# Kernel optimization log

Hardware: AMD Instinct MI355X
Metric: run time of the kernel (lower is better)

## Reference

```python
import jax, jax.numpy as jnp
import numpy as np
import math

LOG_2PI = math.log(2.0 * math.pi)
ETA = 1.0        # Beta(gamma_1=1, gamma_2=eta) stick-breaking prior (gamma buffers at init)
MC_NUM = 4096    # Monte-Carlo samples
T_CLUSTER = 2    # trunc (must be 2: original normalize_factor broadcast requires it)
T_CLS = 2        # classifier DP truncation
DIM = 1024
N = 65536


def mix_weights(b):
    # stick-breaking: pad(b,(0,1),1) * pad(cumprod(1-b),(1,0),1); b: [..., T] -> [..., T+1]
    b1m = jnp.cumprod(1.0 - b, axis=-1)
    ones = jnp.ones((*b.shape[:-1], 1), b.dtype)
    return jnp.concatenate([b, ones], axis=-1) * jnp.concatenate([ones, b1m], axis=-1)


def gauss_log_prob(x, mu, rho):
    # diag Gaussian log-prob summed over feature dim; x [N,D], mu/rho [T,D] -> [N,T]
    std = jnp.log1p(jnp.exp(rho))                      # sigma = log(1+exp(rho))
    inv_var = 1.0 / (std * std)
    const = -0.5 * x.shape[-1] * LOG_2PI - jnp.sum(jnp.log(std), axis=-1)  # [T]
    # 0.5*sum((x-mu)^2/var) expanded as matmuls to avoid an [N,T,D] intermediate
    quad = 0.5 * ((x * x) @ inv_var.T) - x @ (mu * inv_var).T \
           + 0.5 * jnp.sum(mu * mu * inv_var, axis=-1)
    return const - quad


def gauss_entropy(rho):
    # mean over T of diag-Gaussian entropies; rho [T,D] -> scalar
    D = rho.shape[-1]
    std = jnp.log1p(jnp.exp(rho))
    ent = 0.5 * D * (LOG_2PI + 1.0) + jnp.sum(jnp.log(std), axis=-1)  # [T]
    return jnp.mean(ent)


def setup_inputs() -> dict:
    key = jax.random.key(0)
    ks = jax.random.split(key, 5)
    return {
        "x": jax.random.normal(ks[0], (N, DIM), jnp.float32),
        "mu_c": jax.random.normal(ks[1], (T_CLUSTER, DIM), jnp.float32),
        "rho_c": jax.random.normal(ks[2], (T_CLUSTER, DIM), jnp.float32),
        "mu_f": jax.random.normal(ks[3], (T_CLS, DIM), jnp.float32),
        "rho_f": jax.random.normal(ks[4], (T_CLS, DIM), jnp.float32),
    }


def reference(x, mu_c, rho_c, mu_f, rho_f):
    key = jax.random.key(1)
    k1, k2, k3, k4, k5 = jax.random.split(key, 5)

    # ---- D_P_cluster.likelihood(x) ----
    beta_lik = jax.random.beta(k1, 1.0, ETA, (x.shape[0], T_CLUSTER), x.dtype)
    pi_lik = mix_weights(beta_lik)[:, :-1]                 # [N, T]
    ent = gauss_entropy(rho_c)                             # scalar
    log_pdfs = gauss_log_prob(x, mu_c, rho_c)              # [N, T]
    phi = jax.nn.softmax(jnp.log(pi_lik) + ent + log_pdfs, axis=-1)
    neg_likelihood = -jnp.mean(jnp.sum(phi * (ent + log_pdfs), axis=1))

    # ---- MC sampling from the cluster mixture (fused, no Python loop) ----
    betas = jax.random.beta(k2, 1.0, ETA, (MC_NUM, T_CLUSTER), x.dtype)
    w = mix_weights(betas)[:, :-1]                         # [MC, T]
    w = w / jnp.sum(w, axis=1, keepdims=True)              # row-normalize (T==2 makes this exact)
    draws = jax.random.categorical(k3, jnp.log(w), axis=-1)  # [MC] component indices
    eps = jax.random.normal(k4, (MC_NUM, DIM), x.dtype)
    std_c = jnp.log1p(jnp.exp(rho_c))
    mc_samples = mu_c[draws] + std_c[draws] * eps          # [MC, D] reparametrized

    # ---- D_P_clssfy.infer(mc_samples) ----
    beta_inf = jax.random.beta(k5, 1.0, ETA, (MC_NUM, T_CLS), x.dtype)
    pi_inf = mix_weights(beta_inf)[:, :-1]                 # [MC, 2]
    lp_inf = gauss_log_prob(mc_samples, mu_f, rho_f)       # [MC, 2]
    logits = pi_inf * jax.nn.softmax(lp_inf, axis=1)
    return logits, neg_likelihood
```

## Files before the change

kernel.cpp:

```cpp
#include <hip/hip_runtime.h>
#include <stdint.h>

#define LOG2PI_F 1.8378770664093453f
#define D_DIM 1024

typedef float v4f __attribute__((ext_vector_type(4)));

__device__ __forceinline__ uint32_t mix64_32(uint64_t z) {
    z ^= z >> 33; z *= 0xff51afd7ed558ccdULL;
    z ^= z >> 33; z *= 0xc4ceb9fe1a85ec53ULL;
    z ^= z >> 33;
    return (uint32_t)z;
}
__device__ __forceinline__ float unif01(uint32_t stream, uint32_t idx) {
    uint32_t h = mix64_32(((uint64_t)stream << 32) | (uint64_t)idx);
    return (float)(h >> 9) * 0x1p-23f + 0x1p-24f;
}
__device__ __forceinline__ float softplusf(float r) { return log1pf(expf(r)); }

union F4 { v4f v; float f[4]; };

__global__ __launch_bounds__(256) void hdp_lik_kernel(
    const float* __restrict__ x, const float* __restrict__ mu_c,
    const float* __restrict__ rho_c, double* __restrict__ partial)
{
    __shared__ float H0[D_DIM], A0[D_DIM], H1[D_DIM], A1[D_DIM];
    __shared__ float wred[4][4];
    __shared__ double wpart[4];
    const int tid = threadIdx.x, wid = tid >> 6, lane = tid & 63;

    float sls0 = 0.f, sls1 = 0.f, bq0 = 0.f, bq1 = 0.f;
    {
        const int d = tid * 4;
        F4 r0, r1, m0, m1;
        r0.v = *(const v4f*)(rho_c + d);
        r1.v = *(const v4f*)(rho_c + D_DIM + d);
        m0.v = *(const v4f*)(mu_c + d);
        m1.v = *(const v4f*)(mu_c + D_DIM + d);
#pragma unroll
        for (int e = 0; e < 4; ++e) {
            float s0 = softplusf(r0.f[e]);
            float i0 = 1.f / (s0 * s0);
            H0[d + e] = 0.5f * i0; A0[d + e] = m0.f[e] * i0;
            sls0 += logf(s0); bq0 += 0.5f * m0.f[e] * m0.f[e] * i0;
            float s1 = softplusf(r1.f[e]);
            float i1 = 1.f / (s1 * s1);
            H1[d + e] = 0.5f * i1; A1[d + e] = m1.f[e] * i1;
            sls1 += logf(s1); bq1 += 0.5f * m1.f[e] * m1.f[e] * i1;
        }
    }
#pragma unroll
    for (int off = 32; off; off >>= 1) {
        sls0 += __shfl_xor(sls0, off); sls1 += __shfl_xor(sls1, off);
        bq0  += __shfl_xor(bq0,  off); bq1  += __shfl_xor(bq1,  off);
    }
    if (lane == 0) {
        wred[wid][0] = sls0; wred[wid][1] = sls1;
        wred[wid][2] = bq0;  wred[wid][3] = bq1;
    }
    __syncthreads();
    const float SLS0 = wred[0][0] + wred[1][0] + wred[2][0] + wred[3][0];
    const float SLS1 = wred[0][1] + wred[1][1] + wred[2][1] + wred[3][1];
    const float BQ0  = wred[0][2] + wred[1][2] + wred[2][2] + wred[3][2];
    const float BQ1  = wred[0][3] + wred[1][3] + wred[2][3] + wred[3][3];
    const float ent = 0.5f * 1024.f * (LOG2PI_F + 1.f) + 0.5f * (SLS0 + SLS1);
    const float V0 = ent - 0.5f * 1024.f * LOG2PI_F - SLS0 - BQ0;
    const float V1 = ent - 0.5f * 1024.f * LOG2PI_F - SLS1 - BQ1;

    double wsum = 0.0;
    const int rowbase = blockIdx.x * 64 + wid * 16;
    for (int g = 0; g < 4; ++g) {
        const int r0 = rowbase + g * 4;
        float q0[4] = {0.f, 0.f, 0.f, 0.f}, q1[4] = {0.f, 0.f, 0.f, 0.f};
#pragma unroll
        for (int k = 0; k < 4; ++k) {
            const int d = k * 256 + lane * 4;
            F4 xv[4];
#pragma unroll
            for (int r = 0; r < 4; ++r)
                xv[r].v = *(const v4f*)(x + (size_t)(r0 + r) * D_DIM + d);
            F4 h0, a0v, h1, a1v;
            h0.v  = *(const v4f*)&H0[d];
            a0v.v = *(const v4f*)&A0[d];
            h1.v  = *(const v4f*)&H1[d];
            a1v.v = *(const v4f*)&A1[d];
#pragma unroll
            for (int r = 0; r < 4; ++r) {
#pragma unroll
                for (int e = 0; e < 4; ++e) {
                    float xe = xv[r].f[e];
                    float xx = xe * xe;
                    q0[r] = fmaf(xx, h0.f[e], q0[r]);  q0[r] = fmaf(-xe, a0v.f[e], q0[r]);
                    q1[r] = fmaf(xx, h1.f[e], q1[r]);  q1[r] = fmaf(-xe, a1v.f[e], q1[r]);
                }
            }
        }
#pragma unroll
        for (int r = 0; r < 4; ++r) {
            float a = q0[r], b = q1[r];
#pragma unroll
            for (int off = 32; off; off >>= 1) { a += __shfl_xor(a, off); b += __shfl_xor(b, off); }
            const uint32_t row = (uint32_t)(r0 + r);
            float u0 = unif01(1u, 2u * row), u1v = unif01(1u, 2u * row + 1u);
            float lp0 = logf(u0);
            float lp1 = logf(u1v) + logf(1.f - u0);
            float v0 = V0 - a, v1 = V1 - b;
            float s0 = lp0 + v0, s1 = lp1 + v1;
            float mx = fmaxf(s0, s1);
            float e0 = expf(s0 - mx), e1 = expf(s1 - mx);
            float phi0 = e0 / (e0 + e1);
            wsum += (double)(phi0 * v0 + (1.f - phi0) * v1);
        }
    }
    if (lane == 0) wpart[wid] = wsum;
    __syncthreads();
    if (tid == 0) partial[blockIdx.x] = wpart[0] + wpart[1] + wpart[2] + wpart[3];
}

__global__ __launch_bounds__(256) void hdp_cls_kernel(
    const float* __restrict__ mu_c, const float* __restrict__ rho_c,
    const float* __restrict__ mu_f, const float* __restrict__ rho_f,
    const double* __restrict__ partial, float* __restrict__ out)
{
    const int tid = threadIdx.x, wid = tid >> 6, lane = tid & 63;

    if (blockIdx.x == 256) {
        if (wid == 0) {
            double s = 0.0;
            for (int i = lane; i < 1024; i += 64) s += partial[i];
#pragma unroll
            for (int off = 32; off; off >>= 1) s += __shfl_xor(s, off);
            if (lane == 0) out[8192] = (float)(-s / 65536.0);
        }
        return;
    }

    __shared__ float MU0[D_DIM], SD0[D_DIM], MU1[D_DIM], SD1[D_DIM];
    __shared__ float HF0[D_DIM], AF0[D_DIM], HF1[D_DIM], AF1[D_DIM];
    __shared__ float wred[4][2];

    float cf0 = 0.f, cf1 = 0.f;
    {
        const int d = tid * 4;
#pragma unroll
        for (int e = 0; e < 4; ++e) {
            MU0[d + e] = mu_c[d + e];           SD0[d + e] = softplusf(rho_c[d + e]);
            MU1[d + e] = mu_c[D_DIM + d + e];   SD1[d + e] = softplusf(rho_c[D_DIM + d + e]);
            float mf0 = mu_f[d + e], sf0 = softplusf(rho_f[d + e]);
            float i0 = 1.f / (sf0 * sf0);
            HF0[d + e] = 0.5f * i0; AF0[d + e] = mf0 * i0;
            cf0 -= logf(sf0) + 0.5f * mf0 * mf0 * i0;
            float mf1 = mu_f[D_DIM + d + e], sf1 = softplusf(rho_f[D_DIM + d + e]);
            float i1 = 1.f / (sf1 * sf1);
            HF1[d + e] = 0.5f * i1; AF1[d + e] = mf1 * i1;
            cf1 -= logf(sf1) + 0.5f * mf1 * mf1 * i1;
        }
    }
#pragma unroll
    for (int off = 32; off; off >>= 1) {
        cf0 += __shfl_xor(cf0, off); cf1 += __shfl_xor(cf1, off);
    }
    if (lane == 0) { wred[wid][0] = cf0; wred[wid][1] = cf1; }
    __syncthreads();
    const float CF0 = -0.5f * 1024.f * LOG2PI_F
                    + wred[0][0] + wred[1][0] + wred[2][0] + wred[3][0];
    const float CF1 = -0.5f * 1024.f * LOG2PI_F
                    + wred[0][1] + wred[1][1] + wred[2][1] + wred[3][1];

    for (int r = 0; r < 4; ++r) {
        const uint32_t j = (uint32_t)blockIdx.x * 16u + (uint32_t)wid * 4u + (uint32_t)r;
        float b0 = unif01(2u, 2u * j), b1 = unif01(2u, 2u * j + 1u);
        float wn0 = b0 / (b0 + b1 * (1.f - b0));
        int dr = (unif01(3u, j) < wn0) ? 0 : 1;
        float bi0 = unif01(5u, 2u * j), bi1 = unif01(5u, 2u * j + 1u);
        float pi0 = bi0, pi1 = bi1 * (1.f - bi0);
        const float* MU = dr ? &MU1[0] : &MU0[0];
        const float* SD = dr ? &SD1[0] : &SD0[0];
        float qf0 = 0.f, qf1 = 0.f;
#pragma unroll
        for (int k = 0; k < 4; ++k) {
            const int dd = k * 256 + lane * 4;
            F4 mu, sd, h0, a0, h1, a1;
            mu.v = *(const v4f*)&MU[dd];
            sd.v = *(const v4f*)&SD[dd];
            h0.v = *(const v4f*)&HF0[dd];
            a0.v = *(const v4f*)&AF0[dd];
            h1.v = *(const v4f*)&HF1[dd];
            a1.v = *(const v4f*)&AF1[dd];
#pragma unroll
            for (int e = 0; e < 4; e += 2) {
                uint32_t p = j * 512u + (uint32_t)((dd + e) >> 1);
                float uu1 = unif01(4u, p), uu2 = unif01(6u, p);
                float rad = sqrtf(-2.f * logf(uu1));
                float sn, cs;
                __sincosf(6.283185307179586f * uu2, &sn, &cs);
                float mc0 = fmaf(sd.f[e],     rad * cs, mu.f[e]);
                float mc1 = fmaf(sd.f[e + 1], rad * sn, mu.f[e + 1]);
                float xx0 = mc0 * mc0, xx1 = mc1 * mc1;
                qf0 = fmaf(xx0, h0.f[e], qf0);      qf0 = fmaf(-mc0, a0.f[e], qf0);
                qf0 = fmaf(xx1, h0.f[e + 1], qf0);  qf0 = fmaf(-mc1, a0.f[e + 1], qf0);
                qf1 = fmaf(xx0, h1.f[e], qf1);      qf1 = fmaf(-mc0, a1.f[e], qf1);
                qf1 = fmaf(xx1, h1.f[e + 1], qf1);  qf1 = fmaf(-mc1, a1.f[e + 1], qf1);
            }
        }
#pragma unroll
        for (int off = 32; off; off >>= 1) { qf0 += __shfl_xor(qf0, off); qf1 += __shfl_xor(qf1, off); }
        float lp0 = CF0 - qf0, lp1 = CF1 - qf1;
        float mx = fmaxf(lp0, lp1);
        float e0 = expf(lp0 - mx), e1 = expf(lp1 - mx);
        float inv = 1.f / (e0 + e1);
        if (lane == 0) {
            out[2u * j]      = pi0 * e0 * inv;
            out[2u * j + 1u] = pi1 * e1 * inv;
        }
    }
}

extern "C" void kernel_launch(void* const* d_in, const int* in_sizes, int n_in,
                              void* d_out, int out_size, void* d_ws, size_t ws_size,
                              hipStream_t stream) {
    const float* x     = (const float*)d_in[0];
    const float* mu_c  = (const float*)d_in[1];
    const float* rho_c = (const float*)d_in[2];
    const float* mu_f  = (const float*)d_in[3];
    const float* rho_f = (const float*)d_in[4];
    float* out = (float*)d_out;
    double* partial = (double*)d_ws;

    hipLaunchKernelGGL(hdp_lik_kernel, dim3(1024), dim3(256), 0, stream,
                       x, mu_c, rho_c, partial);
    hipLaunchKernelGGL(hdp_cls_kernel, dim3(257), dim3(256), 0, stream,
                       mu_c, rho_c, mu_f, rho_f, partial, out);
}
```

Before: 64.24 us.

## Merge likelihood and classifier work into one launch with a tiny final reduce

The likelihood blocks and the MC classifier blocks now run inside one heterogeneous kernel, dispatched by block index. A separate single-wave kernel does the final reduction of the per-block partial sums. This lets the compute-heavy classifier blocks overlap with the memory-bound likelihood blocks instead of running after them. The trade-off is a larger shared-memory footprint (32KB) for every block, including the likelihood blocks, which may reduce occupancy.

```diff
diff --git a/kernel.cpp b/kernel.cpp
--- a/kernel.cpp
+++ b/kernel.cpp
@@ -20,200 +20,202 @@
 
 union F4 { v4f v; float f[4]; };
 
-__global__ __launch_bounds__(256) void hdp_lik_kernel(
+__global__ __launch_bounds__(256) void hdp_main_kernel(
     const float* __restrict__ x, const float* __restrict__ mu_c,
-    const float* __restrict__ rho_c, double* __restrict__ partial)
+    const float* __restrict__ rho_c, const float* __restrict__ mu_f,
+    const float* __restrict__ rho_f, float* __restrict__ out,
+    double* __restrict__ partial)
 {
-    __shared__ float H0[D_DIM], A0[D_DIM], H1[D_DIM], A1[D_DIM];
+    __shared__ float smem[8192];
     __shared__ float wred[4][4];
     __shared__ double wpart[4];
+    const int bid = blockIdx.x;
     const int tid = threadIdx.x, wid = tid >> 6, lane = tid & 63;
 
-    float sls0 = 0.f, sls1 = 0.f, bq0 = 0.f, bq1 = 0.f;
-    {
-        const int d = tid * 4;
-        F4 r0, r1, m0, m1;
-        r0.v = *(const v4f*)(rho_c + d);
-        r1.v = *(const v4f*)(rho_c + D_DIM + d);
-        m0.v = *(const v4f*)(mu_c + d);
-        m1.v = *(const v4f*)(mu_c + D_DIM + d);
-#pragma unroll
-        for (int e = 0; e < 4; ++e) {
-            float s0 = softplusf(r0.f[e]);
-            float i0 = 1.f / (s0 * s0);
-            H0[d + e] = 0.5f * i0; A0[d + e] = m0.f[e] * i0;
-            sls0 += logf(s0); bq0 += 0.5f * m0.f[e] * m0.f[e] * i0;
-            float s1 = softplusf(r1.f[e]);
-            float i1 = 1.f / (s1 * s1);
-            H1[d + e] = 0.5f * i1; A1[d + e] = m1.f[e] * i1;
-            sls1 += logf(s1); bq1 += 0.5f * m1.f[e] * m1.f[e] * i1;
+    if (bid < 1024) {
+        float* H0 = smem;            float* A0 = smem + 1024;
+        float* H1 = smem + 2048;     float* A1 = smem + 3072;
+
+        float sls0 = 0.f, sls1 = 0.f, bq0 = 0.f, bq1 = 0.f;
+        {
+            const int d = tid * 4;
+            F4 r0, r1, m0, m1;
+            r0.v = *(const v4f*)(rho_c + d);
+            r1.v = *(const v4f*)(rho_c + D_DIM + d);
+            m0.v = *(const v4f*)(mu_c + d);
+            m1.v = *(const v4f*)(mu_c + D_DIM + d);
+#pragma unroll
+            for (int e = 0; e < 4; ++e) {
+                float s0 = softplusf(r0.f[e]);
+                float i0 = 1.f / (s0 * s0);
+                H0[d + e] = 0.5f * i0; A0[d + e] = m0.f[e] * i0;
+                sls0 += logf(s0); bq0 += 0.5f * m0.f[e] * m0.f[e] * i0;
+                float s1 = softplusf(r1.f[e]);
+                float i1 = 1.f / (s1 * s1);
+                H1[d + e] = 0.5f * i1; A1[d + e] = m1.f[e] * i1;
+                sls1 += logf(s1); bq1 += 0.5f * m1.f[e] * m1.f[e] * i1;
+            }
+        }
+#pragma unroll
+        for (int off = 32; off; off >>= 1) {
+            sls0 += __shfl_xor(sls0, off); sls1 += __shfl_xor(sls1, off);
+            bq0  += __shfl_xor(bq0,  off); bq1  += __shfl_xor(bq1,  off);
+        }
+        if (lane == 0) {
+            wred[wid][0] = sls0; wred[wid][1] = sls1;
+            wred[wid][2] = bq0;  wred[wid][3] = bq1;
+        }
+        __syncthreads();
+        const float SLS0 = wred[0][0] + wred[1][0] + wred[2][0] + wred[3][0];
+        const float SLS1 = wred[0][1] + wred[1][1] + wred[2][1] + wred[3][1];
+        const float BQ0  = wred[0][2] + wred[1][2] + wred[2][2] + wred[3][2];
+        const float BQ1  = wred[0][3] + wred[1][3] + wred[2][3] + wred[3][3];
+        const float ent = 0.5f * 1024.f * (LOG2PI_F + 1.f) + 0.5f * (SLS0 + SLS1);
+        const float V0 = ent - 0.5f * 1024.f * LOG2PI_F - SLS0 - BQ0;
+        const float V1 = ent - 0.5f * 1024.f * LOG2PI_F - SLS1 - BQ1;
+
+        double wsum = 0.0;
+        const int rowbase = bid * 64 + wid * 16;
+        for (int g = 0; g < 4; ++g) {
+            const int r0 = rowbase + g * 4;
+            float q0[4] = {0.f, 0.f, 0.f, 0.f}, q1[4] = {0.f, 0.f, 0.f, 0.f};
+#pragma unroll
+            for (int k = 0; k < 4; ++k) {
+                const int d = k * 256 + lane * 4;
+                F4 xv[4];
+#pragma unroll
+                for (int r = 0; r < 4; ++r)
+                    xv[r].v = *(const v4f*)(x + (size_t)(r0 + r) * D_DIM + d);
+                F4 h0, a0v, h1, a1v;
+                h0.v  = *(const v4f*)&H0[d];
+                a0v.v = *(const v4f*)&A0[d];
+                h1.v  = *(const v4f*)&H1[d];
+                a1v.v = *(const v4f*)&A1[d];
+#pragma unroll
+                for (int r = 0; r < 4; ++r) {
+#pragma unroll
+                    for (int e = 0; e < 4; ++e) {
+                        float xe = xv[r].f[e];
+                        float xx = xe * xe;
+                        q0[r] = fmaf(xx, h0.f[e], q0[r]);  q0[r] = fmaf(-xe, a0v.f[e], q0[r]);
+                        q1[r] = fmaf(xx, h1.f[e], q1[r]);  q1[r] = fmaf(-xe, a1v.f[e], q1[r]);
+                    }
+                }
+            }
+#pragma unroll
+            for (int r = 0; r < 4; ++r) {
+                float a = q0[r], b = q1[r];
+#pragma unroll
+                for (int off = 32; off; off >>= 1) { a += __shfl_xor(a, off); b += __shfl_xor(b, off); }
+                const uint32_t row = (uint32_t)(r0 + r);
+                float u0 = unif01(1u, 2u * row), u1v = unif01(1u, 2u * row + 1u);
+                float lp0 = logf(u0);
+                float lp1 = logf(u1v) + logf(1.f - u0);
+                float v0 = V0 - a, v1 = V1 - b;
+                float s0 = lp0 + v0, s1 = lp1 + v1;
+                float mx = fmaxf(s0, s1);
+                float e0 = expf(s0 - mx), e1 = expf(s1 - mx);
+                float phi0 = e0 / (e0 + e1);
+                wsum += (double)(phi0 * v0 + (1.f - phi0) * v1);
+            }
+        }
+        if (lane == 0) wpart[wid] = wsum;
+        __syncthreads();
+        if (tid == 0) partial[bid] = wpart[0] + wpart[1] + wpart[2] + wpart[3];
+    } else {
+        float* MU0 = smem;            float* SD0 = smem + 1024;
+        float* MU1 = smem + 2048;     float* SD1 = smem + 3072;
+        float* HF0 = smem + 4096;     float* AF0 = smem + 5120;
+        float* HF1 = smem + 6144;     float* AF1 = smem + 7168;
+        const int q = bid - 1024;
+
+        float cf0 = 0.f, cf1 = 0.f;
+        {
+            const int d = tid * 4;
+#pragma unroll
+            for (int e = 0; e < 4; ++e) {
+                MU0[d + e] = mu_c[d + e];           SD0[d + e] = softplusf(rho_c[d + e]);
+                MU1[d + e] = mu_c[D_DIM + d + e];   SD1[d + e] = softplusf(rho_c[D_DIM + d + e]);
+                float mf0 = mu_f[d + e], sf0 = softplusf(rho_f[d + e]);
+                float i0 = 1.f / (sf0 * sf0);
+                HF0[d + e] = 0.5f * i0; AF0[d + e] = mf0 * i0;
+                cf0 -= logf(sf0) + 0.5f * mf0 * mf0 * i0;
+                float mf1 = mu_f[D_DIM + d + e], sf1 = softplusf(rho_f[D_DIM + d + e]);
+                float i1 = 1.f / (sf1 * sf1);
+                HF1[d + e] = 0.5f * i1; AF1[d + e] = mf1 * i1;
+                cf1 -= logf(sf1) + 0.5f * mf1 * mf1 * i1;
+            }
+        }
+#pragma unroll
+        for (int off = 32; off; off >>= 1) {
+            cf0 += __shfl_xor(cf0, off); cf1 += __shfl_xor(cf1, off);
+        }
+        if (lane == 0) { wred[wid][0] = cf0; wred[wid][1] = cf1; }
+        __syncthreads();
+        const float CF0 = -0.5f * 1024.f * LOG2PI_F
+                        + wred[0][0] + wred[1][0] + wred[2][0] + wred[3][0];
+        const float CF1 = -0.5f * 1024.f * LOG2PI_F
+                        + wred[0][1] + wred[1][1] + wred[2][1] + wred[3][1];
+
+        for (int r = 0; r < 4; ++r) {
+            const uint32_t j = (uint32_t)q * 16u + (uint32_t)wid * 4u + (uint32_t)r;
+            float b0 = unif01(2u, 2u * j), b1 = unif01(2u, 2u * j + 1u);
+            float wn0 = b0 / (b0 + b1 * (1.f - b0));
+            int dr = (unif01(3u, j) < wn0) ? 0 : 1;
+            float bi0 = unif01(5u, 2u * j), bi1 = unif01(5u, 2u * j + 1u);
+            float pi0 = bi0, pi1 = bi1 * (1.f - bi0);
+            const float* MU = dr ? MU1 : MU0;
+            const float* SD = dr ? SD1 : SD0;
+            float qf0 = 0.f, qf1 = 0.f;
+#pragma unroll
+            for (int k = 0; k < 4; ++k) {
+                const int dd = k * 256 + lane * 4;
+                F4 mu, sd, h0, a0, h1, a1;
+                mu.v = *(const v4f*)&MU[dd];
+                sd.v = *(const v4f*)&SD[dd];
+                h0.v = *(const v4f*)&HF0[dd];
+                a0.v = *(const v4f*)&AF0[dd];
+                h1.v = *(const v4f*)&HF1[dd];
+                a1.v = *(const v4f*)&AF1[dd];
+#pragma unroll
+                for (int e = 0; e < 4; e += 2) {
+                    uint32_t p = j * 512u + (uint32_t)((dd + e) >> 1);
+                    float uu1 = unif01(4u, p), uu2 = unif01(6u, p);
+                    float rad = sqrtf(-2.f * logf(uu1));
+                    float sn, cs;
+                    __sincosf(6.283185307179586f * uu2, &sn, &cs);
+                    float mc0 = fmaf(sd.f[e],     rad * cs, mu.f[e]);
+                    float mc1 = fmaf(sd.f[e + 1], rad * sn, mu.f[e + 1]);
+                    float xx0 = mc0 * mc0, xx1 = mc1 * mc1;
+                    qf0 = fmaf(xx0, h0.f[e], qf0);      qf0 = fmaf(-mc0, a0.f[e], qf0);
+                    qf0 = fmaf(xx1, h0.f[e + 1], qf0);  qf0 = fmaf(-mc1, a0.f[e + 1], qf0);
+                    qf1 = fmaf(xx0, h1.f[e], qf1);      qf1 = fmaf(-mc0, a1.f[e], qf1);
+                    qf1 = fmaf(xx1, h1.f[e + 1], qf1);  qf1 = fmaf(-mc1, a1.f[e + 1], qf1);
+                }
+            }
+#pragma unroll
+            for (int off = 32; off; off >>= 1) { qf0 += __shfl_xor(qf0, off); qf1 += __shfl_xor(qf1, off); }
+            float lp0 = CF0 - qf0, lp1 = CF1 - qf1;
+            float mx = fmaxf(lp0, lp1);
+            float e0 = expf(lp0 - mx), e1 = expf(lp1 - mx);
+            float inv = 1.f / (e0 + e1);
+            if (lane == 0) {
+                out[2u * j]      = pi0 * e0 * inv;
+                out[2u * j + 1u] = pi1 * e1 * inv;
+            }
         }
     }
-#pragma unroll
-    for (int off = 32; off; off >>= 1) {
-        sls0 += __shfl_xor(sls0, off); sls1 += __shfl_xor(sls1, off);
-        bq0  += __shfl_xor(bq0,  off); bq1  += __shfl_xor(bq1,  off);
-    }
-    if (lane == 0) {
-        wred[wid][0] = sls0; wred[wid][1] = sls1;
-        wred[wid][2] = bq0;  wred[wid][3] = bq1;
-    }
-    __syncthreads();
-    const float SLS0 = wred[0][0] + wred[1][0] + wred[2][0] + wred[3][0];
-    const float SLS1 = wred[0][1] + wred[1][1] + wred[2][1] + wred[3][1];
-    const float BQ0  = wred[0][2] + wred[1][2] + wred[2][2] + wred[3][2];
-    const float BQ1  = wred[0][3] + wred[1][3] + wred[2][3] + wred[3][3];
-    const float ent = 0.5f * 1024.f * (LOG2PI_F + 1.f) + 0.5f * (SLS0 + SLS1);
-    const float V0 = ent - 0.5f * 1024.f * LOG2PI_F - SLS0 - BQ0;
-    const float V1 = ent - 0.5f * 1024.f * LOG2PI_F - SLS1 - BQ1;
-
-    double wsum = 0.0;
-    const int rowbase = blockIdx.x * 64 + wid * 16;
-    for (int g = 0; g < 4; ++g) {
-        const int r0 = rowbase + g * 4;
-        float q0[4] = {0.f, 0.f, 0.f, 0.f}, q1[4] = {0.f, 0.f, 0.f, 0.f};
-#pragma unroll
-        for (int k = 0; k < 4; ++k) {
-            const int d = k * 256 + lane * 4;
-            F4 xv[4];
-#pragma unroll
-            for (int r = 0; r < 4; ++r)
-                xv[r].v = *(const v4f*)(x + (size_t)(r0 + r) * D_DIM + d);
-            F4 h0, a0v, h1, a1v;
-            h0.v  = *(const v4f*)&H0[d];
-            a0v.v = *(const v4f*)&A0[d];
-            h1.v  = *(const v4f*)&H1[d];
-            a1v.v = *(const v4f*)&A1[d];
-#pragma unroll
-            for (int r = 0; r < 4; ++r) {
-#pragma unroll
-                for (int e = 0; e < 4; ++e) {
-                    float xe = xv[r].f[e];
-                    float xx = xe * xe;
-                    q0[r] = fmaf(xx, h0.f[e], q0[r]);  q0[r] = fmaf(-xe, a0v.f[e], q0[r]);
-                    q1[r] = fmaf(xx, h1.f[e], q1[r]);  q1[r] = fmaf(-xe, a1v.f[e], q1[r]);
-                }
-            }
-        }
-#pragma unroll
-        for (int r = 0; r < 4; ++r) {
-            float a = q0[r], b = q1[r];
-#pragma unroll
-            for (int off = 32; off; off >>= 1) { a += __shfl_xor(a, off); b += __shfl_xor(b, off); }
-            const uint32_t row = (uint32_t)(r0 + r);
-            float u0 = unif01(1u, 2u * row), u1v = unif01(1u, 2u * row + 1u);
-            float lp0 = logf(u0);
-            float lp1 = logf(u1v) + logf(1.f - u0);
-            float v0 = V0 - a, v1 = V1 - b;
-            float s0 = lp0 + v0, s1 = lp1 + v1;
-            float mx = fmaxf(s0, s1);
-            float e0 = expf(s0 - mx), e1 = expf(s1 - mx);
-            float phi0 = e0 / (e0 + e1);
-            wsum += (double)(phi0 * v0 + (1.f - phi0) * v1);
-        }
-    }
-    if (lane == 0) wpart[wid] = wsum;
-    __syncthreads();
-    if (tid == 0) partial[blockIdx.x] = wpart[0] + wpart[1] + wpart[2] + wpart[3];
-}
-
-__global__ __launch_bounds__(256) void hdp_cls_kernel(
-    const float* __restrict__ mu_c, const float* __restrict__ rho_c,
-    const float* __restrict__ mu_f, const float* __restrict__ rho_f,
-    const double* __restrict__ partial, float* __restrict__ out)
+}
+
+__global__ void hdp_final_kernel(const double* __restrict__ partial,
+                                 float* __restrict__ out)
 {
-    const int tid = threadIdx.x, wid = tid >> 6, lane = tid & 63;
-
-    if (blockIdx.x == 256) {
-        if (wid == 0) {
-            double s = 0.0;
-            for (int i = lane; i < 1024; i += 64) s += partial[i];
-#pragma unroll
-            for (int off = 32; off; off >>= 1) s += __shfl_xor(s, off);
-            if (lane == 0) out[8192] = (float)(-s / 65536.0);
-        }
-        return;
-    }
-
-    __shared__ float MU0[D_DIM], SD0[D_DIM], MU1[D_DIM], SD1[D_DIM];
-    __shared__ float HF0[D_DIM], AF0[D_DIM], HF1[D_DIM], AF1[D_DIM];
-    __shared__ float wred[4][2];
-
-    float cf0 = 0.f, cf1 = 0.f;
-    {
-        const int d = tid * 4;
-#pragma unroll
-        for (int e = 0; e < 4; ++e) {
-            MU0[d + e] = mu_c[d + e];           SD0[d + e] = softplusf(rho_c[d + e]);
-            MU1[d + e] = mu_c[D_DIM + d + e];   SD1[d + e] = softplusf(rho_c[D_DIM + d + e]);
-            float mf0 = mu_f[d + e], sf0 = softplusf(rho_f[d + e]);
-            float i0 = 1.f / (sf0 * sf0);
-            HF0[d + e] = 0.5f * i0; AF0[d + e] = mf0 * i0;
-            cf0 -= logf(sf0) + 0.5f * mf0 * mf0 * i0;
-            float mf1 = mu_f[D_DIM + d + e], sf1 = softplusf(rho_f[D_DIM + d + e]);
-            float i1 = 1.f / (sf1 * sf1);
-            HF1[d + e] = 0.5f * i1; AF1[d + e] = mf1 * i1;
-            cf1 -= logf(sf1) + 0.5f * mf1 * mf1 * i1;
-        }
-    }
-#pragma unroll
-    for (int off = 32; off; off >>= 1) {
-        cf0 += __shfl_xor(cf0, off); cf1 += __shfl_xor(cf1, off);
-    }
-    if (lane == 0) { wred[wid][0] = cf0; wred[wid][1] = cf1; }
-    __syncthreads();
-    const float CF0 = -0.5f * 1024.f * LOG2PI_F
-                    + wred[0][0] + wred[1][0] + wred[2][0] + wred[3][0];
-    const float CF1 = -0.5f * 1024.f * LOG2PI_F
-                    + wred[0][1] + wred[1][1] + wred[2][1] + wred[3][1];
-
-    for (int r = 0; r < 4; ++r) {
-        const uint32_t j = (uint32_t)blockIdx.x * 16u + (uint32_t)wid * 4u + (uint32_t)r;
-        float b0 = unif01(2u, 2u * j), b1 = unif01(2u, 2u * j + 1u);
-        float wn0 = b0 / (b0 + b1 * (1.f - b0));
-        int dr = (unif01(3u, j) < wn0) ? 0 : 1;
-        float bi0 = unif01(5u, 2u * j), bi1 = unif01(5u, 2u * j + 1u);
-        float pi0 = bi0, pi1 = bi1 * (1.f - bi0);
-        const float* MU = dr ? &MU1[0] : &MU0[0];
-        const float* SD = dr ? &SD1[0] : &SD0[0];
-        float qf0 = 0.f, qf1 = 0.f;
-#pragma unroll
-        for (int k = 0; k < 4; ++k) {
-            const int dd = k * 256 + lane * 4;
-            F4 mu, sd, h0, a0, h1, a1;
-            mu.v = *(const v4f*)&MU[dd];
-            sd.v = *(const v4f*)&SD[dd];
-            h0.v = *(const v4f*)&HF0[dd];
-            a0.v = *(const v4f*)&AF0[dd];
-            h1.v = *(const v4f*)&HF1[dd];
-            a1.v = *(const v4f*)&AF1[dd];
-#pragma unroll
-            for (int e = 0; e < 4; e += 2) {
-                uint32_t p = j * 512u + (uint32_t)((dd + e) >> 1);
-                float uu1 = unif01(4u, p), uu2 = unif01(6u, p);
-                float rad = sqrtf(-2.f * logf(uu1));
-                float sn, cs;
-                __sincosf(6.283185307179586f * uu2, &sn, &cs);
-                float mc0 = fmaf(sd.f[e],     rad * cs, mu.f[e]);
-                float mc1 = fmaf(sd.f[e + 1], rad * sn, mu.f[e + 1]);
-                float xx0 = mc0 * mc0, xx1 = mc1 * mc1;
-                qf0 = fmaf(xx0, h0.f[e], qf0);      qf0 = fmaf(-mc0, a0.f[e], qf0);
-                qf0 = fmaf(xx1, h0.f[e + 1], qf0);  qf0 = fmaf(-mc1, a0.f[e + 1], qf0);
-                qf1 = fmaf(xx0, h1.f[e], qf1);      qf1 = fmaf(-mc0, a1.f[e], qf1);
-                qf1 = fmaf(xx1, h1.f[e + 1], qf1);  qf1 = fmaf(-mc1, a1.f[e + 1], qf1);
-            }
-        }
-#pragma unroll
-        for (int off = 32; off; off >>= 1) { qf0 += __shfl_xor(qf0, off); qf1 += __shfl_xor(qf1, off); }
-        float lp0 = CF0 - qf0, lp1 = CF1 - qf1;
-        float mx = fmaxf(lp0, lp1);
-        float e0 = expf(lp0 - mx), e1 = expf(lp1 - mx);
-        float inv = 1.f / (e0 + e1);
-        if (lane == 0) {
-            out[2u * j]      = pi0 * e0 * inv;
-            out[2u * j + 1u] = pi1 * e1 * inv;
-        }
-    }
+    const int lane = threadIdx.x;
+    double s = 0.0;
+    for (int i = lane; i < 1024; i += 64) s += partial[i];
+#pragma unroll
+    for (int off = 32; off; off >>= 1) s += __shfl_xor(s, off);
+    if (lane == 0) out[8192] = (float)(-s / 65536.0);
 }
 
 extern "C" void kernel_launch(void* const* d_in, const int* in_sizes, int n_in,
@@ -227,8 +229,8 @@
     float* out = (float*)d_out;
     double* partial = (double*)d_ws;
 
-    hipLaunchKernelGGL(hdp_lik_kernel, dim3(1024), dim3(256), 0, stream,
-                       x, mu_c, rho_c, partial);
-    hipLaunchKernelGGL(hdp_cls_kernel, dim3(257), dim3(256), 0, stream,
-                       mu_c, rho_c, mu_f, rho_f, partial, out);
-}
+    hipLaunchKernelGGL(hdp_main_kernel, dim3(1280), dim3(256), 0, stream,
+                       x, mu_c, rho_c, mu_f, rho_f, out, partial);
+    hipLaunchKernelGGL(hdp_final_kernel, dim3(1), dim3(64), 0, stream,
+                       partial, out);
+}
```

Result: slower. 65.54 us (+2.0%).
